# Kernel optimization log

Measured on AMD Instinct MI355X. Metric: run time of the kernel, lower is better.

The kernel has to match this reference:

```python
import jax, jax.numpy as jnp
import numpy as np

EPS_FEAT = 1e-4   # stabilizer eps inside favorp_projection
EPS_DEN = 0.01    # clamp_min eps for the attention denominator


def favorp_projection(data, projection_matrix, is_query):
    # data: [b, h, n, d]; projection_matrix: [h, m, d]
    d = data.shape[-1]
    data_normalizer = d ** (-0.25)
    ratio = projection_matrix.shape[1] ** (-0.5)
    data_dash = jnp.einsum('bhnd,hmd->bhnm', data_normalizer * data, projection_matrix)
    diag_data = (jnp.sum(data * data, axis=-1) * 0.5 * data_normalizer * data_normalizer)[..., None]
    if is_query:
        stabilizer = jax.lax.stop_gradient(jnp.max(data_dash, axis=-1, keepdims=True))
    else:
        stabilizer = jax.lax.stop_gradient(jnp.max(data_dash, axis=(-1, -2), keepdims=True))
    return ratio * jnp.exp(data_dash - diag_data - stabilizer) + EPS_FEAT


def setup_inputs() -> dict:
    key = jax.random.key(0)
    ks = jax.random.split(key, 12)
    N, B, E, H, D, M = 4096, 4, 1024, 16, 64, 64
    s = E ** -0.5
    return {
        'query': jax.random.normal(ks[0], (N, B, E), jnp.float32),
        'key': jax.random.normal(ks[1], (N, B, E), jnp.float32),
        'value': jax.random.normal(ks[2], (N, B, E), jnp.float32),
        'Wq': jax.random.normal(ks[3], (E, E), jnp.float32) * s,
        'bq': jax.random.normal(ks[4], (E,), jnp.float32) * 0.02,
        'Wk': jax.random.normal(ks[5], (E, E), jnp.float32) * s,
        'bk': jax.random.normal(ks[6], (E,), jnp.float32) * 0.02,
        'Wv': jax.random.normal(ks[7], (E, E), jnp.float32) * s,
        'bv': jax.random.normal(ks[8], (E,), jnp.float32) * 0.02,
        'Wo': jax.random.normal(ks[9], (E, E), jnp.float32) * s,
        'bo': jax.random.normal(ks[10], (E,), jnp.float32) * 0.02,
        'proj': jax.random.normal(ks[11], (H, M, D), jnp.float32),
    }


def reference(query, key, value, Wq, bq, Wk, bk, Wv, bv, Wo, bo, proj):
    H = proj.shape[0]
    # [n, b, e] -> [b, n, e]
    q_in = query.transpose(1, 0, 2)
    k_in = key.transpose(1, 0, 2)
    v_in = value.transpose(1, 0, 2)
    B, N, E = q_in.shape
    D = E // H

    def lin(x, W, b):
        return jnp.einsum('bne,fe->bnf', x, W) + b

    def split_heads(x):  # [b, n, e] -> [b, h, n, d]
        return x.reshape(B, N, H, D).transpose(0, 2, 1, 3)

    q = split_heads(lin(q_in, Wq, bq))
    k = split_heads(lin(k_in, Wk, bk))
    v = split_heads(lin(v_in, Wv, bv))

    q_prime = favorp_projection(q, proj, is_query=True)   # [b, h, n, m]
    k_prime = favorp_projection(k, proj, is_query=False)  # [b, h, n, m]

    # non-causal linear attention: O(n * m * d)
    kv = jnp.einsum('bhnm,bhnd->bhmd', k_prime, v)
    qkv = jnp.einsum('bhnm,bhmd->bhnd', q_prime, kv)
    normalizer = jnp.einsum('bhnm,bhm->bhn', q_prime, k_prime.sum(axis=2))
    output = qkv / jnp.maximum(normalizer[..., None], EPS_DEN)

    attn_output = output.transpose(0, 2, 1, 3).reshape(B, N, E)  # b h n d -> b n (h d)
    out = lin(attn_output, Wo, bo)
    return out.transpose(1, 0, 2)  # back to [n, b, e]
```

## Files before the change

kernel.cpp:

```cpp
#include <hip/hip_runtime.h>
#include <math.h>

#define B_   4
#define N_   4096
#define E_   1024
#define H_   16
#define BN_  (B_*N_)
#define BH_  (B_*H_)
#define SPLITK 8

#define NRM_C   0.35355339059327373f
#define DIAG_C  0.0625f
#define RATIO_C 0.125f
#define EPSF    1e-4f
#define EPSD    0.01f

typedef __attribute__((ext_vector_type(8))) short bf16x8;
typedef __attribute__((ext_vector_type(4))) float f32x4;

__device__ __forceinline__ unsigned short f32_to_bf16(float x) {
    unsigned int u = __float_as_uint(x);
    unsigned int r = (u + 0x7fffu + ((u >> 16) & 1u)) >> 16;
    return (unsigned short)r;
}
__device__ __forceinline__ float bf16_to_f32(unsigned short h) {
    return __uint_as_float(((unsigned int)h) << 16);
}

__device__ __forceinline__ void atomicMaxF(float* addr, float v) {
    if (v >= 0.f) atomicMax((int*)addr, __float_as_int(v));
    else          atomicMin((unsigned int*)addr, __float_as_uint(v));
}

__global__ void init_stab(float* stab) {
    if (threadIdx.x < BH_) stab[threadIdx.x] = -INFINITY;
}

template<int IN_MODE>
__global__ __launch_bounds__(256) void convert_split(const float* __restrict__ src,
                                                     unsigned short* __restrict__ hi,
                                                     unsigned short* __restrict__ lo,
                                                     int total4)
{
    int i = blockIdx.x * 256 + threadIdx.x;
    const int stride = gridDim.x * 256;
    for (; i < total4; i += stride) {
        long e4 = (long)i * 4;
        const float* p;
        if (IN_MODE == 0) {
            long r = e4 >> 10; int e = (int)(e4 & 1023);
            int b = (int)(r >> 12), n = (int)(r & 4095);
            p = src + (((long)(n * B_ + b)) << 10) + e;
        } else {
            p = src + e4;
        }
        float4 v = *(const float4*)p;
        ushort4 h, l;
        h.x = f32_to_bf16(v.x); l.x = f32_to_bf16(v.x - bf16_to_f32(h.x));
        h.y = f32_to_bf16(v.y); l.y = f32_to_bf16(v.y - bf16_to_f32(h.y));
        h.z = f32_to_bf16(v.z); l.z = f32_to_bf16(v.z - bf16_to_f32(h.z));
        h.w = f32_to_bf16(v.w); l.w = f32_to_bf16(v.w - bf16_to_f32(h.w));
        *(ushort4*)(hi + e4) = h;
        *(ushort4*)(lo + e4) = l;
    }
}

__device__ __forceinline__ void gl_lds16(const unsigned short* g, unsigned short* l) {
    __builtin_amdgcn_global_load_lds((const __attribute__((address_space(1))) void*)g,
                                     (__attribute__((address_space(3))) void*)l, 16, 0, 0);
}

template<int OUT_MODE>
__global__ __launch_bounds__(256) void gemm_mfma(const unsigned short* __restrict__ Ahi,
                                                 const unsigned short* __restrict__ Alo,
                                                 const unsigned short* __restrict__ Bhi,
                                                 const unsigned short* __restrict__ Blo,
                                                 const float* __restrict__ bias,
                                                 float* __restrict__ Y)
{
    __shared__ __align__(16) unsigned short smem[2 * 4 * 4096];
    const int t = threadIdx.x;
    const int w = t >> 6, lane = t & 63;
    const int row0 = blockIdx.x * 128, col0 = blockIdx.y * 128;
    const int wrow = (w >> 1) * 64, wcol = (w & 1) * 64;
    const int g = lane >> 4, rl = lane & 15;

    const int sr = w * 32 + (lane >> 2);
    const int kswz = (((lane & 3) ^ ((lane >> 2) & 3)) << 3);
    const long aoff = (long)(row0 + sr) * E_ + kswz;
    const long boff = (long)(col0 + sr) * E_ + kswz;

    f32x4 acc[4][4];
#pragma unroll
    for (int m = 0; m < 4; ++m)
#pragma unroll
        for (int n = 0; n < 4; ++n) acc[m][n] = (f32x4){0.f, 0.f, 0.f, 0.f};

#define STAGE_STEP(KS, BUF)                                                          \
    {                                                                                \
        const int k0 = (KS) * 32;                                                    \
        unsigned short* d = smem + (BUF) * 16384 + w * 1024;                         \
        gl_lds16(Ahi + aoff + k0,             d);                                    \
        gl_lds16(Ahi + aoff + k0 + 16 * E_,   d + 512);                              \
        gl_lds16(Alo + aoff + k0,             d + 4096);                             \
        gl_lds16(Alo + aoff + k0 + 16 * E_,   d + 4096 + 512);                       \
        gl_lds16(Bhi + boff + k0,             d + 8192);                             \
        gl_lds16(Bhi + boff + k0 + 16 * E_,   d + 8192 + 512);                       \
        gl_lds16(Blo + boff + k0,             d + 12288);                            \
        gl_lds16(Blo + boff + k0 + 16 * E_,   d + 12288 + 512);                      \
    }

    STAGE_STEP(0, 0);

    for (int ks = 0; ks < 32; ++ks) {
        __syncthreads();
        if (ks + 1 < 32) STAGE_STEP(ks + 1, (ks + 1) & 1);
        const unsigned short* sb = smem + (ks & 1) * 16384;
        bf16x8 ah[4], al[4], bh[4], bl[4];
#pragma unroll
        for (int m = 0; m < 4; ++m) {
            int r = wrow + m * 16 + rl;
            int off = r * 32 + ((g ^ (r & 3)) << 3);
            ah[m] = *(const bf16x8*)(sb + off);
            al[m] = *(const bf16x8*)(sb + 4096 + off);
        }
#pragma unroll
        for (int n = 0; n < 4; ++n) {
            int r = wcol + n * 16 + rl;
            int off = r * 32 + ((g ^ (r & 3)) << 3);
            bh[n] = *(const bf16x8*)(sb + 8192 + off);
            bl[n] = *(const bf16x8*)(sb + 12288 + off);
        }
#pragma unroll
        for (int m = 0; m < 4; ++m)
#pragma unroll
            for (int n = 0; n < 4; ++n)
                acc[m][n] = __builtin_amdgcn_mfma_f32_16x16x32_bf16(ah[m], bh[n], acc[m][n], 0, 0, 0);
#pragma unroll
        for (int m = 0; m < 4; ++m)
#pragma unroll
            for (int n = 0; n < 4; ++n)
                acc[m][n] = __builtin_amdgcn_mfma_f32_16x16x32_bf16(ah[m], bl[n], acc[m][n], 0, 0, 0);
#pragma unroll
        for (int m = 0; m < 4; ++m)
#pragma unroll
            for (int n = 0; n < 4; ++n)
                acc[m][n] = __builtin_amdgcn_mfma_f32_16x16x32_bf16(al[m], bh[n], acc[m][n], 0, 0, 0);
    }
#undef STAGE_STEP

    float bv[4];
#pragma unroll
    for (int n = 0; n < 4; ++n) bv[n] = bias[col0 + wcol + n * 16 + rl];
#pragma unroll
    for (int m = 0; m < 4; ++m) {
        int rbase = row0 + wrow + m * 16 + g * 4;
#pragma unroll
        for (int n = 0; n < 4; ++n) {
            int c = col0 + wcol + n * 16 + rl;
#pragma unroll
            for (int q = 0; q < 4; ++q) {
                int r = rbase + q;
                float v = acc[m][n][q] + bv[n];
                long off;
                if (OUT_MODE == 0) off = (long)r * E_ + c;
                else { int b = r >> 12, nn = r & (N_ - 1); off = (long)(nn * B_ + b) * E_ + c; }
                Y[off] = v;
            }
        }
    }
}

template<int IN_MODE, int OUT_MODE>
__global__ __launch_bounds__(256) void lin_gemm(const float* __restrict__ X,
                                                const float* __restrict__ W,
                                                const float* __restrict__ bias,
                                                float* __restrict__ Y)
{
    __shared__ float As[16][68];
    __shared__ float Ws[16][68];
    const int row0 = blockIdx.x * 64;
    const int col0 = blockIdx.y * 64;
    const int t  = threadIdx.x;
    const int lr = t >> 2;
    const int lk = (t & 3) * 4;
    const int ty = t >> 4, tx = t & 15;

    long arow;
    {
        int r = row0 + lr;
        if (IN_MODE == 0) { int b = r >> 12, n = r & (N_ - 1); arow = (long)(n * B_ + b) * E_; }
        else              { arow = (long)r * E_; }
    }
    const long wrow = (long)(col0 + lr) * E_;

    float acc[4][4] = {};
    for (int e0 = 0; e0 < E_; e0 += 16) {
        float4 av = *(const float4*)(X + arow + e0 + lk);
        float4 wv = *(const float4*)(W + wrow + e0 + lk);
        As[lk+0][lr] = av.x; As[lk+1][lr] = av.y; As[lk+2][lr] = av.z; As[lk+3][lr] = av.w;
        Ws[lk+0][lr] = wv.x; Ws[lk+1][lr] = wv.y; Ws[lk+2][lr] = wv.z; Ws[lk+3][lr] = wv.w;
        __syncthreads();
#pragma unroll
        for (int k = 0; k < 16; ++k) {
            float4 a = *(const float4*)&As[k][ty*4];
            float4 w = *(const float4*)&Ws[k][tx*4];
            float a_[4] = {a.x,a.y,a.z,a.w};
            float w_[4] = {w.x,w.y,w.z,w.w};
#pragma unroll
            for (int i = 0; i < 4; ++i)
#pragma unroll
                for (int j = 0; j < 4; ++j)
                    acc[i][j] = fmaf(a_[i], w_[j], acc[i][j]);
        }
        __syncthreads();
    }
    float4 bvv = *(const float4*)(bias + col0 + tx*4);
    float b_[4] = {bvv.x,bvv.y,bvv.z,bvv.w};
#pragma unroll
    for (int i = 0; i < 4; ++i) {
        int r = row0 + ty*4 + i;
        float4 o;
        o.x = acc[i][0] + b_[0]; o.y = acc[i][1] + b_[1];
        o.z = acc[i][2] + b_[2]; o.w = acc[i][3] + b_[3];
        long off;
        if (OUT_MODE == 0) off = (long)r * E_ + col0 + tx*4;
        else { int b = r >> 12, n = r & (N_ - 1); off = (long)(n * B_ + b) * E_ + col0 + tx*4; }
        *(float4*)(Y + off) = o;
    }
}

template<int IS_QUERY>
__global__ __launch_bounds__(256) void favorp_dash(float* __restrict__ Xh,
                                                   const float* __restrict__ proj,
                                                   float* __restrict__ stab)
{
    __shared__ float Xs[64][68];
    __shared__ float Ps[64][68];
    __shared__ float diag[64];
    __shared__ float red4[4];
    __shared__ float rowred[64][17];
    const int bh = blockIdx.x, b = bh >> 4, h = bh & 15;
    const int n0 = blockIdx.y * 64;
    const int t = threadIdx.x;
    const int r = t >> 2, c0 = (t & 3) * 16;
    const int ty = t >> 4, tx = t & 15;

    const float* xrow = Xh + (long)(b * N_ + n0 + r) * E_ + h * 64;
    const float* prow = proj + (long)(h * 64 + r) * 64;
#pragma unroll
    for (int c = 0; c < 4; ++c) {
        float4 v = *(const float4*)(xrow + c0 + c*4);
        Xs[c0+c*4+0][r] = v.x; Xs[c0+c*4+1][r] = v.y; Xs[c0+c*4+2][r] = v.z; Xs[c0+c*4+3][r] = v.w;
        float4 p = *(const float4*)(prow + c0 + c*4);
        Ps[c0+c*4+0][r] = p.x; Ps[c0+c*4+1][r] = p.y; Ps[c0+c*4+2][r] = p.z; Ps[c0+c*4+3][r] = p.w;
    }
    __syncthreads();
    if (t < 64) {
        float s = 0.f;
#pragma unroll 16
        for (int d = 0; d < 64; ++d) { float x = Xs[d][t]; s = fmaf(x, x, s); }
        diag[t] = s * DIAG_C;
    }
    __syncthreads();

    float acc[4][4] = {};
#pragma unroll 16
    for (int d = 0; d < 64; ++d) {
        float4 a = *(const float4*)&Xs[d][ty*4];
        float4 p = *(const float4*)&Ps[d][tx*4];
        float a_[4] = {a.x,a.y,a.z,a.w};
        float p_[4] = {p.x,p.y,p.z,p.w};
#pragma unroll
        for (int i = 0; i < 4; ++i)
#pragma unroll
            for (int j = 0; j < 4; ++j)
                acc[i][j] = fmaf(a_[i], p_[j], acc[i][j]);
    }
    float dash[4][4];
#pragma unroll
    for (int i = 0; i < 4; ++i)
#pragma unroll
        for (int j = 0; j < 4; ++j) dash[i][j] = acc[i][j] * NRM_C;

    if (IS_QUERY) {
#pragma unroll
        for (int i = 0; i < 4; ++i) {
            float m = fmaxf(fmaxf(dash[i][0], dash[i][1]), fmaxf(dash[i][2], dash[i][3]));
            rowred[ty*4+i][tx] = m;
        }
        __syncthreads();
#pragma unroll
        for (int i = 0; i < 4; ++i) {
            int row = ty*4 + i;
            float m = rowred[row][0];
#pragma unroll
            for (int jj = 1; jj < 16; ++jj) m = fmaxf(m, rowred[row][jj]);
            float dg = diag[row];
            float4 o;
            o.x = RATIO_C * expf(dash[i][0] - dg - m) + EPSF;
            o.y = RATIO_C * expf(dash[i][1] - dg - m) + EPSF;
            o.z = RATIO_C * expf(dash[i][2] - dg - m) + EPSF;
            o.w = RATIO_C * expf(dash[i][3] - dg - m) + EPSF;
            *(float4*)(Xh + (long)(b * N_ + n0 + row) * E_ + h * 64 + tx*4) = o;
        }
    } else {
        float lmax = dash[0][0];
#pragma unroll
        for (int i = 0; i < 4; ++i)
#pragma unroll
            for (int j = 0; j < 4; ++j) lmax = fmaxf(lmax, dash[i][j]);
#pragma unroll
        for (int i = 0; i < 4; ++i) {
            int row = ty*4 + i;
            float dg = diag[row];
            float4 o = { dash[i][0]-dg, dash[i][1]-dg, dash[i][2]-dg, dash[i][3]-dg };
            *(float4*)(Xh + (long)(b * N_ + n0 + row) * E_ + h * 64 + tx*4) = o;
        }
#pragma unroll
        for (int off = 32; off > 0; off >>= 1) lmax = fmaxf(lmax, __shfl_down(lmax, off));
        if ((t & 63) == 0) red4[t >> 6] = lmax;
        __syncthreads();
        if (t == 0)
            atomicMaxF(&stab[bh], fmaxf(fmaxf(red4[0], red4[1]), fmaxf(red4[2], red4[3])));
    }
}

__global__ __launch_bounds__(256) void kv_partial(const float* __restrict__ T1,
                                                  const float* __restrict__ V,
                                                  const float* __restrict__ stab,
                                                  float* __restrict__ kvp,
                                                  float* __restrict__ ksump)
{
    __shared__ float KPs[16][68];
    __shared__ float Vs[16][68];
    const int bh = blockIdx.x, chunk = blockIdx.y;
    const int b = bh >> 4, h = bh & 15;
    const int t = threadIdx.x;
    const int lr = t >> 4, lm = (t & 15) * 4;
    const int ty = t >> 4, tx = t & 15;
    const float stb = stab[bh];
    float acc[4][4] = {};
    float ks = 0.f;
    const int nbeg = chunk * (N_ / SPLITK), nend = nbeg + (N_ / SPLITK);
    for (int n0 = nbeg; n0 < nend; n0 += 16) {
        long rowoff = (long)(b * N_ + n0 + lr) * E_ + h * 64 + lm;
        float4 tv = *(const float4*)(T1 + rowoff);
        float4 vv = *(const float4*)(V + rowoff);
        KPs[lr][lm+0] = RATIO_C * expf(tv.x - stb) + EPSF;
        KPs[lr][lm+1] = RATIO_C * expf(tv.y - stb) + EPSF;
        KPs[lr][lm+2] = RATIO_C * expf(tv.z - stb) + EPSF;
        KPs[lr][lm+3] = RATIO_C * expf(tv.w - stb) + EPSF;
        *(float4*)&Vs[lr][lm] = vv;
        __syncthreads();
        if (t < 64) {
#pragma unroll
            for (int rr = 0; rr < 16; ++rr) ks += KPs[rr][t];
        }
#pragma unroll
        for (int k = 0; k < 16; ++k) {
            float4 a = *(const float4*)&KPs[k][ty*4];
            float4 v4 = *(const float4*)&Vs[k][tx*4];
            float a_[4] = {a.x,a.y,a.z,a.w};
            float v_[4] = {v4.x,v4.y,v4.z,v4.w};
#pragma unroll
            for (int i = 0; i < 4; ++i)
#pragma unroll
                for (int j = 0; j < 4; ++j)
                    acc[i][j] = fmaf(a_[i], v_[j], acc[i][j]);
        }
        __syncthreads();
    }
    const long kvbase = ((long)chunk * BH_ + bh) * 4096;
#pragma unroll
    for (int i = 0; i < 4; ++i) {
        float4 o = {acc[i][0], acc[i][1], acc[i][2], acc[i][3]};
        *(float4*)(kvp + kvbase + (ty*4+i) * 64 + tx*4) = o;
    }
    if (t < 64) ksump[((long)chunk * BH_ + bh) * 64 + t] = ks;
}

__global__ __launch_bounds__(256) void kv_reduce(const float* __restrict__ kvp,
                                                 const float* __restrict__ ksump,
                                                 float* __restrict__ kv,
                                                 float* __restrict__ ksum)
{
    int idx = blockIdx.x * 256 + threadIdx.x;
    if (idx < BH_ * 4096) {
        float s = 0.f;
#pragma unroll
        for (int c = 0; c < SPLITK; ++c) s += kvp[(long)c * BH_ * 4096 + idx];
        kv[idx] = s;
    } else {
        int j = idx - BH_ * 4096;
        if (j < BH_ * 64) {
            float s = 0.f;
#pragma unroll
            for (int c = 0; c < SPLITK; ++c) s += ksump[(long)c * BH_ * 64 + j];
            ksum[j] = s;
        }
    }
}

template<int SPLIT>
__global__ __launch_bounds__(256) void qkv_attn(const float* __restrict__ Qp,
                                                const float* __restrict__ kvM,
                                                const float* __restrict__ ksum,
                                                float* __restrict__ attn,
                                                unsigned short* __restrict__ Ohi,
                                                unsigned short* __restrict__ Olo)
{
    __shared__ float QPs[64][68];
    __shared__ float kvs[64][68];
    __shared__ float ksums[64];
    __shared__ float rnorm[64];
    const int bh = blockIdx.x, b = bh >> 4, h = bh & 15;
    const int n0 = blockIdx.y * 64;
    const int t = threadIdx.x;
    const int r = t >> 2, c0 = (t & 3) * 16;
    const int ty = t >> 4, tx = t & 15;

#pragma unroll
    for (int c = 0; c < 4; ++c) {
        int idx = t * 16 + c * 4;
        float4 v = *(const float4*)(kvM + (long)bh * 4096 + idx);
        *(float4*)&kvs[idx >> 6][idx & 63] = v;
    }
    if (t < 64) ksums[t] = ksum[bh * 64 + t];
    const float* qrow = Qp + (long)(b * N_ + n0 + r) * E_ + h * 64;
#pragma unroll
    for (int c = 0; c < 4; ++c) {
        float4 v = *(const float4*)(qrow + c0 + c*4);
        QPs[c0+c*4+0][r] = v.x; QPs[c0+c*4+1][r] = v.y; QPs[c0+c*4+2][r] = v.z; QPs[c0+c*4+3][r] = v.w;
    }
    __syncthreads();
    if (t < 64) {
        float s = 0.f;
#pragma unroll 16
        for (int m = 0; m < 64; ++m) s = fmaf(QPs[m][t], ksums[m], s);
        rnorm[t] = 1.f / fmaxf(s, EPSD);
    }
    __syncthreads();
    float acc[4][4] = {};
#pragma unroll 16
    for (int m = 0; m < 64; ++m) {
        float4 a = *(const float4*)&QPs[m][ty*4];
        float4 v4 = *(const float4*)&kvs[m][tx*4];
        float a_[4] = {a.x,a.y,a.z,a.w};
        float v_[4] = {v4.x,v4.y,v4.z,v4.w};
#pragma unroll
        for (int i = 0; i < 4; ++i)
#pragma unroll
            for (int j = 0; j < 4; ++j)
                acc[i][j] = fmaf(a_[i], v_[j], acc[i][j]);
    }
#pragma unroll
    for (int i = 0; i < 4; ++i) {
        int row = ty*4 + i;
        float rn = rnorm[row];
        float4 o = {acc[i][0]*rn, acc[i][1]*rn, acc[i][2]*rn, acc[i][3]*rn};
        if (SPLIT) {
            long off = (((long)(b * N_ + n0 + row)) << 10) + h * 64 + tx * 4;
            ushort4 hh, ll;
            hh.x = f32_to_bf16(o.x); ll.x = f32_to_bf16(o.x - bf16_to_f32(hh.x));
            hh.y = f32_to_bf16(o.y); ll.y = f32_to_bf16(o.y - bf16_to_f32(hh.y));
            hh.z = f32_to_bf16(o.z); ll.z = f32_to_bf16(o.z - bf16_to_f32(hh.z));
            hh.w = f32_to_bf16(o.w); ll.w = f32_to_bf16(o.w - bf16_to_f32(hh.w));
            *(ushort4*)(Ohi + off) = hh;
            *(ushort4*)(Olo + off) = ll;
        } else {
            *(float4*)(attn + (long)(b * N_ + n0 + row) * E_ + h * 64 + tx*4) = o;
        }
    }
}

extern "C" void kernel_launch(void* const* d_in, const int* in_sizes, int n_in,
                              void* d_out, int out_size, void* d_ws, size_t ws_size,
                              hipStream_t stream)
{
    const float* query = (const float*)d_in[0];
    const float* key   = (const float*)d_in[1];
    const float* value = (const float*)d_in[2];
    const float* Wq    = (const float*)d_in[3];
    const float* bq    = (const float*)d_in[4];
    const float* Wk    = (const float*)d_in[5];
    const float* bk    = (const float*)d_in[6];
    const float* Wv    = (const float*)d_in[7];
    const float* bv    = (const float*)d_in[8];
    const float* Wo    = (const float*)d_in[9];
    const float* bo    = (const float*)d_in[10];
    const float* proj  = (const float*)d_in[11];
    float* O = (float*)d_out;

    float* ws = (float*)d_ws;
    const size_t SZ = (size_t)BN_ * E_;
    float* A     = ws;
    float* kvp   = ws + SZ;
    float* ksump = kvp + (size_t)SPLITK * BH_ * 4096;
    float* kvM   = ksump + (size_t)SPLITK * BH_ * 64;
    float* ksum  = kvM + (size_t)BH_ * 4096;
    float* stab  = ksum + (size_t)BH_ * 64;
    const size_t COMMON = SZ + (size_t)SPLITK * BH_ * 4096 + (size_t)SPLITK * BH_ * 64
                        + (size_t)BH_ * 4096 + (size_t)BH_ * 64 + 64;
    unsigned short* Xhi = (unsigned short*)(ws + COMMON);
    unsigned short* Xlo = Xhi + SZ;
    unsigned short* Whi = Xlo + SZ;
    unsigned short* Wlo = Whi + (size_t)E_ * E_;
    const size_t NEED_FAST = (COMMON + SZ + (size_t)E_ * E_) * 4;

    dim3 gF(BH_, N_ / 64);
    dim3 gKV(BH_, SPLITK);
    const int nRed = (BH_ * 4096 + BH_ * 64) / 256;

    if (ws_size >= NEED_FAST) {
        dim3 gG(BN_ / 128, E_ / 128);
        const int X4 = (int)(SZ / 4), W4 = (E_ * E_) / 4;
        convert_split<0><<<2048, 256, 0, stream>>>(key, Xhi, Xlo, X4);
        convert_split<1><<<1024, 256, 0, stream>>>(Wk, Whi, Wlo, W4);
        gemm_mfma<0><<<gG, 256, 0, stream>>>(Xhi, Xlo, Whi, Wlo, bk, O);
        init_stab<<<1, 64, 0, stream>>>(stab);
        favorp_dash<0><<<gF, 256, 0, stream>>>(O, proj, stab);
        convert_split<0><<<2048, 256, 0, stream>>>(value, Xhi, Xlo, X4);
        convert_split<1><<<1024, 256, 0, stream>>>(Wv, Whi, Wlo, W4);
        gemm_mfma<0><<<gG, 256, 0, stream>>>(Xhi, Xlo, Whi, Wlo, bv, A);
        kv_partial<<<gKV, 256, 0, stream>>>(O, A, stab, kvp, ksump);
        kv_reduce<<<nRed, 256, 0, stream>>>(kvp, ksump, kvM, ksum);
        convert_split<0><<<2048, 256, 0, stream>>>(query, Xhi, Xlo, X4);
        convert_split<1><<<1024, 256, 0, stream>>>(Wq, Whi, Wlo, W4);
        gemm_mfma<0><<<gG, 256, 0, stream>>>(Xhi, Xlo, Whi, Wlo, bq, O);
        favorp_dash<1><<<gF, 256, 0, stream>>>(O, proj, stab);
        qkv_attn<1><<<gF, 256, 0, stream>>>(O, kvM, ksum, nullptr, Xhi, Xlo);
        convert_split<1><<<1024, 256, 0, stream>>>(Wo, Whi, Wlo, W4);
        gemm_mfma<1><<<gG, 256, 0, stream>>>(Xhi, Xlo, Whi, Wlo, bo, O);
    } else {
        dim3 gGemm(BN_ / 64, E_ / 64);
        lin_gemm<0,0><<<gGemm, 256, 0, stream>>>(key, Wk, bk, O);
        init_stab<<<1, 64, 0, stream>>>(stab);
        favorp_dash<0><<<gF, 256, 0, stream>>>(O, proj, stab);
        lin_gemm<0,0><<<gGemm, 256, 0, stream>>>(value, Wv, bv, A);
        kv_partial<<<gKV, 256, 0, stream>>>(O, A, stab, kvp, ksump);
        kv_reduce<<<nRed, 256, 0, stream>>>(kvp, ksump, kvM, ksum);
        lin_gemm<0,0><<<gGemm, 256, 0, stream>>>(query, Wq, bq, O);
        favorp_dash<1><<<gF, 256, 0, stream>>>(O, proj, stab);
        qkv_attn<0><<<gF, 256, 0, stream>>>(O, kvM, ksum, A, nullptr, nullptr);
        lin_gemm<1,1><<<gGemm, 256, 0, stream>>>(A, Wo, bo, O);
    }
}
```

Baseline: 667.0 us.

## Fuse FAVOR+ feature projection and attention output into the MFMA projection GEMM epilogues

The K and Q projection GEMMs now stage their output tiles in LDS and run the random-feature projection in the epilogue with split-bf16 MFMAs. This removes the separate favorp_dash kernels and the fp32 round trip of the projected activations. For Q, the epilogue also applies exp, the normalizer and the kv product against a transposed split-bf16 kv, then writes hi/lo bf16 attention output straight into the Wo GEMM input, which removes qkv_attn. In exchange the epilogue uses much more LDS and registers, which may lower occupancy, and it adds error from the split-bf16 matmuls.

Measured after the change: 625.3 us. 1.07x faster.

```diff
diff --git a/kernel.cpp b/kernel.cpp
--- a/kernel.cpp
+++ b/kernel.cpp
@@ -70,15 +70,26 @@
                                      (__attribute__((address_space(3))) void*)l, 16, 0, 0);
 }
 
-template<int OUT_MODE>
+#define SMEM_BYTES (4*64*68*4 + 2*4*64*4)
+
+template<int MODE>
 __global__ __launch_bounds__(256) void gemm_mfma(const unsigned short* __restrict__ Ahi,
                                                  const unsigned short* __restrict__ Alo,
                                                  const unsigned short* __restrict__ Bhi,
                                                  const unsigned short* __restrict__ Blo,
                                                  const float* __restrict__ bias,
-                                                 float* __restrict__ Y)
+                                                 float* __restrict__ Y,
+                                                 float* __restrict__ stab,
+                                                 const unsigned short* __restrict__ PShi,
+                                                 const unsigned short* __restrict__ PSlo,
+                                                 const unsigned short* __restrict__ kvThi,
+                                                 const unsigned short* __restrict__ kvTlo,
+                                                 const float* __restrict__ ksum,
+                                                 unsigned short* __restrict__ AttnHi,
+                                                 unsigned short* __restrict__ AttnLo)
 {
-    __shared__ __align__(16) unsigned short smem[2 * 4 * 4096];
+    __shared__ __align__(16) char SMEM[SMEM_BYTES];
+    unsigned short* smem = (unsigned short*)SMEM;
     const int t = threadIdx.x;
     const int w = t >> 6, lane = t & 63;
     const int row0 = blockIdx.x * 128, col0 = blockIdx.y * 128;
@@ -152,22 +163,176 @@
     float bv[4];
 #pragma unroll
     for (int n = 0; n < 4; ++n) bv[n] = bias[col0 + wcol + n * 16 + rl];
-#pragma unroll
-    for (int m = 0; m < 4; ++m) {
-        int rbase = row0 + wrow + m * 16 + g * 4;
-#pragma unroll
-        for (int n = 0; n < 4; ++n) {
-            int c = col0 + wcol + n * 16 + rl;
+
+    if (MODE <= 1) {
+#pragma unroll
+        for (int m = 0; m < 4; ++m) {
+            int rbase = row0 + wrow + m * 16 + g * 4;
+#pragma unroll
+            for (int n = 0; n < 4; ++n) {
+                int c = col0 + wcol + n * 16 + rl;
+#pragma unroll
+                for (int q = 0; q < 4; ++q) {
+                    int r = rbase + q;
+                    float v = acc[m][n][q] + bv[n];
+                    long off;
+                    if (MODE == 0) off = (long)r * E_ + c;
+                    else { int b = r >> 12, nn = r & (N_ - 1); off = (long)(nn * B_ + b) * E_ + c; }
+                    Y[off] = v;
+                }
+            }
+        }
+        return;
+    }
+
+    __syncthreads();
+    float* accF  = (float*)SMEM + w * (64 * 68);
+    float* diagL = (float*)(SMEM + 4*64*68*4) + w * 64;
+    float* rnmL  = (float*)(SMEM + 4*64*68*4) + 256 + w * 64;
+    const int b_idx = row0 >> 12;
+    const int hg = (col0 >> 6) + (w & 1);
+    const int bh = b_idx * H_ + hg;
+
+#pragma unroll
+    for (int m = 0; m < 4; ++m)
+#pragma unroll
+        for (int n = 0; n < 4; ++n)
+#pragma unroll
+            for (int q = 0; q < 4; ++q)
+                accF[(m*16 + g*4 + q) * 68 + n*16 + rl] = acc[m][n][q] + bv[n];
+    {
+        float s = 0.f;
+#pragma unroll 16
+        for (int d = 0; d < 64; ++d) { float x = accF[lane * 68 + d]; s = fmaf(x, x, s); }
+        diagL[lane] = s * DIAG_C;
+    }
+    __syncthreads();
+
+    float wavemax = -INFINITY;
+#pragma unroll
+    for (int mi = 0; mi < 4; ++mi) {
+        bf16x8 dah[2], dal[2];
+#pragma unroll
+        for (int kk = 0; kk < 2; ++kk) {
+            const float* src = &accF[(mi*16 + rl) * 68 + kk*32 + g*8];
+            float4 f0 = *(const float4*)src, f1 = *(const float4*)(src + 4);
+            float fv[8] = {f0.x,f0.y,f0.z,f0.w,f1.x,f1.y,f1.z,f1.w};
+            bf16x8 hh, ll;
+#pragma unroll
+            for (int j = 0; j < 8; ++j) {
+                unsigned short h16 = f32_to_bf16(fv[j]);
+                hh[j] = (short)h16;
+                ll[j] = (short)f32_to_bf16(fv[j] - bf16_to_f32(h16));
+            }
+            dah[kk] = hh; dal[kk] = ll;
+        }
+        f32x4 dacc[4];
+#pragma unroll
+        for (int n = 0; n < 4; ++n) dacc[n] = (f32x4){0.f,0.f,0.f,0.f};
+#pragma unroll
+        for (int n = 0; n < 4; ++n)
+#pragma unroll
+            for (int kk = 0; kk < 2; ++kk) {
+                long po = (long)hg * 4096 + (n*16 + rl) * 64 + kk*32 + g*8;
+                bf16x8 pbh = *(const bf16x8*)(PShi + po);
+                bf16x8 pbl = *(const bf16x8*)(PSlo + po);
+                dacc[n] = __builtin_amdgcn_mfma_f32_16x16x32_bf16(dah[kk], pbh, dacc[n], 0, 0, 0);
+                dacc[n] = __builtin_amdgcn_mfma_f32_16x16x32_bf16(dah[kk], pbl, dacc[n], 0, 0, 0);
+                dacc[n] = __builtin_amdgcn_mfma_f32_16x16x32_bf16(dal[kk], pbh, dacc[n], 0, 0, 0);
+            }
+        if (MODE == 2) {
+#pragma unroll
+            for (int n = 0; n < 4; ++n)
+#pragma unroll
+                for (int q = 0; q < 4; ++q) {
+                    float dsh = dacc[n][q] * NRM_C;
+                    wavemax = fmaxf(wavemax, dsh);
+                    int rloc = mi*16 + g*4 + q;
+                    Y[(long)(row0 + wrow + rloc) * E_ + col0 + wcol + n*16 + rl] = dsh - diagL[rloc];
+                }
+        } else {
+            float rm0 = -INFINITY, rm1 = -INFINITY, rm2 = -INFINITY, rm3 = -INFINITY;
+#pragma unroll
+            for (int n = 0; n < 4; ++n) {
+                rm0 = fmaxf(rm0, dacc[n][0]); rm1 = fmaxf(rm1, dacc[n][1]);
+                rm2 = fmaxf(rm2, dacc[n][2]); rm3 = fmaxf(rm3, dacc[n][3]);
+            }
+#pragma unroll
+            for (int off = 1; off < 16; off <<= 1) {
+                rm0 = fmaxf(rm0, __shfl_xor(rm0, off));
+                rm1 = fmaxf(rm1, __shfl_xor(rm1, off));
+                rm2 = fmaxf(rm2, __shfl_xor(rm2, off));
+                rm3 = fmaxf(rm3, __shfl_xor(rm3, off));
+            }
+            float rmq[4] = {rm0 * NRM_C, rm1 * NRM_C, rm2 * NRM_C, rm3 * NRM_C};
+#pragma unroll
+            for (int n = 0; n < 4; ++n)
+#pragma unroll
+                for (int q = 0; q < 4; ++q) {
+                    int rloc = mi*16 + g*4 + q;
+                    float qp = RATIO_C * expf(dacc[n][q] * NRM_C - diagL[rloc] - rmq[q]) + EPSF;
+                    accF[rloc * 68 + n*16 + rl] = qp;
+                }
+        }
+    }
+
+    if (MODE == 2) {
+#pragma unroll
+        for (int off = 1; off < 64; off <<= 1) wavemax = fmaxf(wavemax, __shfl_xor(wavemax, off));
+        if (lane == 0) atomicMaxF(&stab[bh], wavemax);
+        return;
+    }
+
+    {
+        float s = 0.f;
+        const float* kb = ksum + bh * 64;
+#pragma unroll 16
+        for (int m = 0; m < 64; ++m) s = fmaf(accF[lane * 68 + m], kb[m], s);
+        rnmL[lane] = 1.f / fmaxf(s, EPSD);
+    }
+    __syncthreads();
+#pragma unroll
+    for (int mi = 0; mi < 4; ++mi) {
+        bf16x8 qah[2], qal[2];
+#pragma unroll
+        for (int kk = 0; kk < 2; ++kk) {
+            const float* src = &accF[(mi*16 + rl) * 68 + kk*32 + g*8];
+            float4 f0 = *(const float4*)src, f1 = *(const float4*)(src + 4);
+            float fv[8] = {f0.x,f0.y,f0.z,f0.w,f1.x,f1.y,f1.z,f1.w};
+            bf16x8 hh, ll;
+#pragma unroll
+            for (int j = 0; j < 8; ++j) {
+                unsigned short h16 = f32_to_bf16(fv[j]);
+                hh[j] = (short)h16;
+                ll[j] = (short)f32_to_bf16(fv[j] - bf16_to_f32(h16));
+            }
+            qah[kk] = hh; qal[kk] = ll;
+        }
+        f32x4 oacc[4];
+#pragma unroll
+        for (int n = 0; n < 4; ++n) oacc[n] = (f32x4){0.f,0.f,0.f,0.f};
+#pragma unroll
+        for (int n = 0; n < 4; ++n)
+#pragma unroll
+            for (int kk = 0; kk < 2; ++kk) {
+                long ko = (long)bh * 4096 + (n*16 + rl) * 64 + kk*32 + g*8;
+                bf16x8 kbh = *(const bf16x8*)(kvThi + ko);
+                bf16x8 kbl = *(const bf16x8*)(kvTlo + ko);
+                oacc[n] = __builtin_amdgcn_mfma_f32_16x16x32_bf16(qah[kk], kbh, oacc[n], 0, 0, 0);
+                oacc[n] = __builtin_amdgcn_mfma_f32_16x16x32_bf16(qah[kk], kbl, oacc[n], 0, 0, 0);
+                oacc[n] = __builtin_amdgcn_mfma_f32_16x16x32_bf16(qal[kk], kbh, oacc[n], 0, 0, 0);
+            }
+#pragma unroll
+        for (int n = 0; n < 4; ++n)
 #pragma unroll
             for (int q = 0; q < 4; ++q) {
-                int r = rbase + q;
-                float v = acc[m][n][q] + bv[n];
-                long off;
-                if (OUT_MODE == 0) off = (long)r * E_ + c;
-                else { int b = r >> 12, nn = r & (N_ - 1); off = (long)(nn * B_ + b) * E_ + c; }
-                Y[off] = v;
+                int rloc = mi*16 + g*4 + q;
+                float o = oacc[n][q] * rnmL[rloc];
+                long off = (long)(row0 + wrow + rloc) * E_ + col0 + wcol + n*16 + rl;
+                unsigned short h16 = f32_to_bf16(o);
+                AttnHi[off] = h16;
+                AttnLo[off] = f32_to_bf16(o - bf16_to_f32(h16));
             }
-        }
     }
 }
 
@@ -382,15 +547,22 @@
 
 __global__ __launch_bounds__(256) void kv_reduce(const float* __restrict__ kvp,
                                                  const float* __restrict__ ksump,
-                                                 float* __restrict__ kv,
-                                                 float* __restrict__ ksum)
+                                                 float* __restrict__ kvM,
+                                                 float* __restrict__ ksum,
+                                                 unsigned short* __restrict__ kvThi,
+                                                 unsigned short* __restrict__ kvTlo)
 {
     int idx = blockIdx.x * 256 + threadIdx.x;
     if (idx < BH_ * 4096) {
         float s = 0.f;
 #pragma unroll
         for (int c = 0; c < SPLITK; ++c) s += kvp[(long)c * BH_ * 4096 + idx];
-        kv[idx] = s;
+        kvM[idx] = s;
+        int bh = idx >> 12, md = idx & 4095, m = md >> 6, d = md & 63;
+        unsigned short h16 = f32_to_bf16(s);
+        long toff = (long)bh * 4096 + d * 64 + m;
+        kvThi[toff] = h16;
+        kvTlo[toff] = f32_to_bf16(s - bf16_to_f32(h16));
     } else {
         int j = idx - BH_ * 4096;
         if (j < BH_ * 64) {
@@ -402,13 +574,10 @@
     }
 }
 
-template<int SPLIT>
 __global__ __launch_bounds__(256) void qkv_attn(const float* __restrict__ Qp,
                                                 const float* __restrict__ kvM,
                                                 const float* __restrict__ ksum,
-                                                float* __restrict__ attn,
-                                                unsigned short* __restrict__ Ohi,
-                                                unsigned short* __restrict__ Olo)
+                                                float* __restrict__ attn)
 {
     __shared__ float QPs[64][68];
     __shared__ float kvs[64][68];
@@ -459,18 +628,7 @@
         int row = ty*4 + i;
         float rn = rnorm[row];
         float4 o = {acc[i][0]*rn, acc[i][1]*rn, acc[i][2]*rn, acc[i][3]*rn};
-        if (SPLIT) {
-            long off = (((long)(b * N_ + n0 + row)) << 10) + h * 64 + tx * 4;
-            ushort4 hh, ll;
-            hh.x = f32_to_bf16(o.x); ll.x = f32_to_bf16(o.x - bf16_to_f32(hh.x));
-            hh.y = f32_to_bf16(o.y); ll.y = f32_to_bf16(o.y - bf16_to_f32(hh.y));
-            hh.z = f32_to_bf16(o.z); ll.z = f32_to_bf16(o.z - bf16_to_f32(hh.z));
-            hh.w = f32_to_bf16(o.w); ll.w = f32_to_bf16(o.w - bf16_to_f32(hh.w));
-            *(ushort4*)(Ohi + off) = hh;
-            *(ushort4*)(Olo + off) = ll;
-        } else {
-            *(float4*)(attn + (long)(b * N_ + n0 + row) * E_ + h * 64 + tx*4) = o;
-        }
+        *(float4*)(attn + (long)(b * N_ + n0 + row) * E_ + h * 64 + tx*4) = o;
     }
 }
 
@@ -500,13 +658,22 @@
     float* kvM   = ksump + (size_t)SPLITK * BH_ * 64;
     float* ksum  = kvM + (size_t)BH_ * 4096;
     float* stab  = ksum + (size_t)BH_ * 64;
+    unsigned short* kvThi = (unsigned short*)(stab + 64);
+    unsigned short* kvTlo = kvThi + (size_t)BH_ * 4096;
+    unsigned short* PShi  = kvTlo + (size_t)BH_ * 4096;
+    unsigned short* PSlo  = PShi + 65536;
     const size_t COMMON = SZ + (size_t)SPLITK * BH_ * 4096 + (size_t)SPLITK * BH_ * 64
-                        + (size_t)BH_ * 4096 + (size_t)BH_ * 64 + 64;
-    unsigned short* Xhi = (unsigned short*)(ws + COMMON);
+                        + (size_t)BH_ * 4096 + (size_t)BH_ * 64 + 64
+                        + ((size_t)BH_ * 4096)  + 65536 / 2 * 2 / 2 * 0 + 32768 * 2 / 2;
+    const size_t EXTRA_F = (size_t)BH_ * 4096  + 65536 ;
+    const size_t COMMON_F = SZ + (size_t)SPLITK * BH_ * 4096 + (size_t)SPLITK * BH_ * 64
+                          + (size_t)BH_ * 4096 + (size_t)BH_ * 64 + 64 + EXTRA_F;
+    unsigned short* Xhi = (unsigned short*)(ws + COMMON_F);
     unsigned short* Xlo = Xhi + SZ;
     unsigned short* Whi = Xlo + SZ;
     unsigned short* Wlo = Whi + (size_t)E_ * E_;
-    const size_t NEED_FAST = (COMMON + SZ + (size_t)E_ * E_) * 4;
+    const size_t NEED_FAST = (COMMON_F + SZ + (size_t)E_ * E_) * 4;
+    (void)COMMON;
 
     dim3 gF(BH_, N_ / 64);
     dim3 gKV(BH_, SPLITK);
@@ -515,23 +682,28 @@
     if (ws_size >= NEED_FAST) {
         dim3 gG(BN_ / 128, E_ / 128);
         const int X4 = (int)(SZ / 4), W4 = (E_ * E_) / 4;
+        unsigned short* AttnHi = (unsigned short*)A;
+        unsigned short* AttnLo = AttnHi + SZ;
+
+        convert_split<1><<<64, 256, 0, stream>>>(proj, PShi, PSlo, 16384);
+        init_stab<<<1, 64, 0, stream>>>(stab);
         convert_split<0><<<2048, 256, 0, stream>>>(key, Xhi, Xlo, X4);
         convert_split<1><<<1024, 256, 0, stream>>>(Wk, Whi, Wlo, W4);
-        gemm_mfma<0><<<gG, 256, 0, stream>>>(Xhi, Xlo, Whi, Wlo, bk, O);
-        init_stab<<<1, 64, 0, stream>>>(stab);
-        favorp_dash<0><<<gF, 256, 0, stream>>>(O, proj, stab);
+        gemm_mfma<2><<<gG, 256, 0, stream>>>(Xhi, Xlo, Whi, Wlo, bk, O, stab,
+                                             PShi, PSlo, nullptr, nullptr, nullptr, nullptr, nullptr);
         convert_split<0><<<2048, 256, 0, stream>>>(value, Xhi, Xlo, X4);
         convert_split<1><<<1024, 256, 0, stream>>>(Wv, Whi, Wlo, W4);
-        gemm_mfma<0><<<gG, 256, 0, stream>>>(Xhi, Xlo, Whi, Wlo, bv, A);
+        gemm_mfma<0><<<gG, 256, 0, stream>>>(Xhi, Xlo, Whi, Wlo, bv, A, nullptr,
+                                             nullptr, nullptr, nullptr, nullptr, nullptr, nullptr, nullptr);
         kv_partial<<<gKV, 256, 0, stream>>>(O, A, stab, kvp, ksump);
-        kv_reduce<<<nRed, 256, 0, stream>>>(kvp, ksump, kvM, ksum);
+        kv_reduce<<<nRed, 256, 0, stream>>>(kvp, ksump, kvM, ksum, kvThi, kvTlo);
         convert_split<0><<<2048, 256, 0, stream>>>(query, Xhi, Xlo, X4);
         convert_split<1><<<1024, 256, 0, stream>>>(Wq, Whi, Wlo, W4);
-        gemm_mfma<0><<<gG, 256, 0, stream>>>(Xhi, Xlo, Whi, Wlo, bq, O);
-        favorp_dash<1><<<gF, 256, 0, stream>>>(O, proj, stab);
-        qkv_attn<1><<<gF, 256, 0, stream>>>(O, kvM, ksum, nullptr, Xhi, Xlo);
+        gemm_mfma<3><<<gG, 256, 0, stream>>>(Xhi, Xlo, Whi, Wlo, bq, nullptr, nullptr,
+                                             PShi, PSlo, kvThi, kvTlo, ksum, AttnHi, AttnLo);
         convert_split<1><<<1024, 256, 0, stream>>>(Wo, Whi, Wlo, W4);
-        gemm_mfma<1><<<gG, 256, 0, stream>>>(Xhi, Xlo, Whi, Wlo, bo, O);
+        gemm_mfma<1><<<gG, 256, 0, stream>>>(AttnHi, AttnLo, Whi, Wlo, bo, O, nullptr,
+                                             nullptr, nullptr, nullptr, nullptr, nullptr, nullptr, nullptr);
     } else {
         dim3 gGemm(BN_ / 64, E_ / 64);
         lin_gemm<0,0><<<gGemm, 256, 0, stream>>>(key, Wk, bk, O);
@@ -539,10 +711,10 @@
         favorp_dash<0><<<gF, 256, 0, stream>>>(O, proj, stab);
         lin_gemm<0,0><<<gGemm, 256, 0, stream>>>(value, Wv, bv, A);
         kv_partial<<<gKV, 256, 0, stream>>>(O, A, stab, kvp, ksump);
-        kv_reduce<<<nRed, 256, 0, stream>>>(kvp, ksump, kvM, ksum);
+        kv_reduce<<<nRed, 256, 0, stream>>>(kvp, ksump, kvM, ksum, kvThi, kvTlo);
         lin_gemm<0,0><<<gGemm, 256, 0, stream>>>(query, Wq, bq, O);
         favorp_dash<1><<<gF, 256, 0, stream>>>(O, proj, stab);
-        qkv_attn<0><<<gF, 256, 0, stream>>>(O, kvM, ksum, A, nullptr, nullptr);
+        qkv_attn<<<gF, 256, 0, stream>>>(O, kvM, ksum, A);
         lin_gemm<1,1><<<gGemm, 256, 0, stream>>>(A, Wo, bo, O);
     }
 }
```
